# Optimization experiments

Hardware: AMD Instinct MI355X
Metric: run time of the kernel (lower is better)

Reference implementation:

```python
import jax, jax.numpy as jnp
import numpy as np

# --- SLAYER hyperparameters (from netParams) ---
THETA = 10.0        # spike threshold
TAU_SR = 10.0       # SRM alpha-kernel time constant (ms)
TAU_RHO = 1.0       # surrogate-gradient width
SCALE_RHO = 1.0     # surrogate-gradient scale
TS = 1.0            # simulation step (ms)
T_SAMPLE = 300      # number of time steps
K_LEN = 64          # truncated SRM kernel length

N_BATCH, N_IN, N_HID, N_OUT = 128, 784, 410, 10


def srm_kernel():
    # SRM-alpha kernel eps(t) = (t/tau) * exp(1 - t/tau), sampled at Ts, eps(0)=0
    t = jnp.arange(K_LEN, dtype=jnp.float32) * TS
    return (t / TAU_SR) * jnp.exp(1.0 - t / TAU_SR)


def psp(x):
    # Causal FIR filtering along time: out[t] = sum_k eps[k] * x[t-k]
    # x: [N, C, T]
    n, c, t = x.shape
    kern = srm_kernel()
    lhs = x.reshape(n * c, 1, t)
    rhs = kern[::-1].reshape(1, 1, K_LEN)  # flip: conv_general_dilated is cross-correlation
    out = jax.lax.conv_general_dilated(
        lhs, rhs, window_strides=(1,), padding=[(K_LEN - 1, 0)],
        dimension_numbers=("NCH", "OIH", "NCH"))
    return out.reshape(n, c, t)


@jax.custom_vjp
def spike_fn(u):
    # Heaviside threshold with surrogate gradient rho(u) = (scale/tau) * exp(-|u-theta|/tau)
    return (u >= THETA).astype(u.dtype)

def _spike_fwd(u):
    return spike_fn(u), u

def _spike_bwd(u, g):
    return (g * (SCALE_RHO / TAU_RHO) * jnp.exp(-jnp.abs(u - THETA) / TAU_RHO),)

spike_fn.defvjp(_spike_fwd, _spike_bwd)


def setup_inputs() -> dict:
    key = jax.random.key(0)
    k1, k2, k3, k4 = jax.random.split(key, 4)
    img = jax.random.uniform(k1, (N_BATCH, N_IN), dtype=jnp.float32)
    rand_u = jax.random.uniform(k2, (N_BATCH, N_IN, T_SAMPLE), dtype=jnp.float32)
    W1 = jax.random.normal(k3, (N_HID, N_IN), dtype=jnp.float32)
    W2 = jax.random.normal(k4, (N_OUT, N_HID), dtype=jnp.float32)
    return {"img": img, "rand_u": rand_u, "W1": W1, "W2": W2}


def reference(img, rand_u, W1, W2):
    # Poisson spike encoding: spike whenever uniform noise < pixel intensity
    s0 = (rand_u < img[:, :, None]).astype(jnp.float32)        # [N, 784, T]
    # fc1 (dense over spatial features, shared over time) -> psp -> spike
    a1 = jnp.einsum("nit,oi->not", s0, W1)                     # [N, 410, T]
    s1 = spike_fn(psp(a1))
    # fc2 -> psp -> spike
    a2 = jnp.einsum("nht,oh->not", s1, W2)                     # [N, 10, T]
    s2 = spike_fn(psp(a2))
    return s2
```

## Files before the change

### kernel.cpp

```cpp
#include <hip/hip_runtime.h>
#include <cstdint>
#include <cstddef>

#define N_B 128
#define N_I 784
#define N_H 410
#define N_O 10
#define TT  300
#define KL  64
#define NW  26
#define NKS 13
#define NTILES 26
#define NDIG 4
#define NKS2 7
#define S1_TILE 4800
#define S1_NSTRIDE 134400

typedef int v4i __attribute__((ext_vector_type(4)));

__device__ __forceinline__ uint32_t expand4(uint32_t v) {
  return (v * 0x00204081u) & 0x01010101u;
}

__global__ void k_pack(const float* __restrict__ rand_u, const float* __restrict__ img,
                       uint32_t* __restrict__ s0w) {
  int n = blockIdx.y;
  int t = blockIdx.x * 64 + threadIdx.x;
  if (t >= TT) return;
  const float* rb = rand_u + (size_t)n * N_I * TT + t;
  const float* ib = img + (size_t)n * N_I;
  uint32_t* dst = s0w + ((size_t)n * TT + t) * NW;
  #pragma unroll 1
  for (int w = 0; w < 25; ++w) {
    int ib32 = w * 32;
    float r[32];
    #pragma unroll
    for (int b = 0; b < 32; ++b) {
      int i = ib32 + b;
      r[b] = (i < N_I) ? rb[(size_t)i * TT] : 2.0f;
    }
    uint32_t bits = 0;
    #pragma unroll
    for (int b = 0; b < 32; ++b) {
      int i = ib32 + b;
      float p = (i < N_I) ? ib[i] : 0.0f;
      bits |= (r[b] < p ? 1u : 0u) << b;
    }
    dst[w] = bits;
  }
  dst[25] = 0;
}

__global__ void k_bprepall(const float* __restrict__ W1, const float* __restrict__ W2,
                           v4i* __restrict__ Bf, v4i* __restrict__ Bf2) {
  int bid  = blockIdx.x;
  int lane = threadIdx.x;
  if (bid < NDIG * NTILES * NKS) {
    int ks   = bid % NKS;
    int rest = bid / NKS;
    int nt   = rest % NTILES;
    int d    = rest / NTILES;
    int o     = nt * 16 + (lane & 15);
    int kbase = ks * 64 + (lane >> 4) * 16;
    uint32_t wds[4] = {0, 0, 0, 0};
    for (int j = 0; j < 16; ++j) {
      int k = kbase + j;
      int dig = 0;
      if (o < N_H && k < N_I) {
        double w = (double)W1[(size_t)o * N_I + k];
        int r = (int)llround(w * 268435456.0);
        for (int dd = 0; dd <= d; ++dd) {
          dig = (int)(int8_t)(uint8_t)(r & 255);
          r = (r - dig) >> 8;
        }
      }
      wds[j >> 2] |= ((uint32_t)(uint8_t)(int8_t)dig) << (8 * (j & 3));
    }
    v4i v; v[0] = (int)wds[0]; v[1] = (int)wds[1]; v[2] = (int)wds[2]; v[3] = (int)wds[3];
    Bf[(size_t)bid * 64 + lane] = v;
  } else {
    int b2 = bid - NDIG * NTILES * NKS;
    int ks = b2 % NKS2, d = b2 / NKS2;
    int o     = lane & 15;
    int kbase = ks * 64 + (lane >> 4) * 16;
    uint32_t wds[4] = {0, 0, 0, 0};
    for (int j = 0; j < 16; ++j) {
      int k = kbase + j;
      int dig = 0;
      if (o < N_O && k < N_H) {
        double w = (double)W2[(size_t)o * N_H + k];
        int r = (int)llround(w * 268435456.0);
        for (int dd = 0; dd <= d; ++dd) {
          dig = (int)(int8_t)(uint8_t)(r & 255);
          r = (r - dig) >> 8;
        }
      }
      wds[j >> 2] |= ((uint32_t)(uint8_t)(int8_t)dig) << (8 * (j & 3));
    }
    v4i v; v[0] = (int)wds[0]; v[1] = (int)wds[1]; v[2] = (int)wds[2]; v[3] = (int)wds[3];
    Bf2[(size_t)b2 * 64 + lane] = v;
  }
}

__global__ __launch_bounds__(256) void k_fused2(const uint32_t* __restrict__ s0w,
                                                const v4i* __restrict__ Bf,
                                                uint8_t* __restrict__ s1) {
  __shared__ double tile[TT][17];
  int tid = threadIdx.x;
  int wave = tid >> 6, lane = tid & 63;
  int nt = blockIdx.x, n = blockIdx.y;
  int lrow = lane & 15, quad = lane >> 4;
  int wsel = quad >> 1, hsel = (quad & 1) * 16;
  const v4i* bb = Bf + (size_t)nt * NKS * 64 + lane;
  const size_t dstr = (size_t)NTILES * NKS * 64;
  const uint32_t* srow = s0w + (size_t)n * TT * NW;

  v4i acc[5][NDIG];
  #pragma unroll
  for (int mti = 0; mti < 5; ++mti)
    #pragma unroll
    for (int d = 0; d < NDIG; ++d) { acc[mti][d][0]=0; acc[mti][d][1]=0; acc[mti][d][2]=0; acc[mti][d][3]=0; }
  int rowc[5];
  #pragma unroll
  for (int mti = 0; mti < 5; ++mti) {
    int rr = wave * 80 + mti * 16 + lrow;
    rowc[mti] = (rr > TT - 1) ? TT - 1 : rr;
  }
  v4i bcur[NDIG]; uint32_t acur[5];
  #pragma unroll
  for (int d = 0; d < NDIG; ++d) bcur[d] = bb[(size_t)d * dstr];
  #pragma unroll
  for (int mti = 0; mti < 5; ++mti) acur[mti] = srow[(size_t)rowc[mti] * NW + wsel];
  for (int ks = 0; ks < NKS; ++ks) {
    int ks2 = (ks + 1 < NKS) ? ks + 1 : ks;
    v4i bnxt[NDIG]; uint32_t anxt[5];
    #pragma unroll
    for (int d = 0; d < NDIG; ++d) bnxt[d] = bb[(size_t)d * dstr + ks2 * 64];
    #pragma unroll
    for (int mti = 0; mti < 5; ++mti) anxt[mti] = srow[(size_t)rowc[mti] * NW + ks2 * 2 + wsel];
    #pragma unroll
    for (int mti = 0; mti < 5; ++mti) {
      uint32_t h = (acur[mti] >> hsel) & 0xFFFFu;
      v4i af;
      af[0] = (int)expand4(h & 0xF);
      af[1] = (int)expand4((h >> 4) & 0xF);
      af[2] = (int)expand4((h >> 8) & 0xF);
      af[3] = (int)expand4((h >> 12) & 0xF);
      #pragma unroll
      for (int d = 0; d < NDIG; ++d)
        acc[mti][d] = __builtin_amdgcn_mfma_i32_16x16x64_i8(af, bcur[d], acc[mti][d], 0, 0, 0);
    }
    #pragma unroll
    for (int d = 0; d < NDIG; ++d) bcur[d] = bnxt[d];
    #pragma unroll
    for (int mti = 0; mti < 5; ++mti) acur[mti] = anxt[mti];
  }
  #pragma unroll
  for (int mti = 0; mti < 5; ++mti)
    #pragma unroll
    for (int r = 0; r < 4; ++r) {
      int m = wave * 80 + mti * 16 + quad * 4 + r;
      if (m < TT) {
        double v = (double)acc[mti][0][r]
                 + 256.0      * (double)acc[mti][1][r]
                 + 65536.0    * (double)acc[mti][2][r]
                 + 16777216.0 * (double)acc[mti][3][r];
        tile[m][lrow] = v;
      }
    }
  __syncthreads();

  if (lane < 16) {
    int g = wave;
    int T0 = g * 75, T1 = T0 + 75;
    int W = T0 - 63; if (W < 0) W = 0;
    int tB = W + 64, tM = (tB < T1) ? tB : T1;
    const double q   = exp(-0.1);
    const double q64 = exp(-6.4);
    const double cS  = (exp(1.0) / 10.0) * (1.0 / 268435456.0);
    double s1a = 0.0, s2a = 0.0, s1b = 0.0, s2b = 0.0;
    uint8_t* sb = s1 + (size_t)n * S1_NSTRIDE + (size_t)nt * S1_TILE + lane;
    for (int t = W; t < T0; ++t) {
      double xa = tile[t][lane];
      s2a = q * (s2a + s1a);
      s1a = q * s1a + xa;
    }
    for (int t = T0; t < tM; ++t) {
      double xa = tile[t][lane];
      s2a = q * (s2a + s1a);
      s1a = q * s1a + xa;
      sb[(size_t)t * 16] = (cS * s2a >= 10.0) ? 1 : 0;
    }
    for (int t = tM; t < T1; ++t) {
      double xb = tile[t - 64][lane];
      double xa = tile[t][lane];
      s2b = q * (s2b + s1b);
      s1b = q * s1b + xb;
      s2a = q * (s2a + s1a);
      s1a = q * s1a + xa;
      double y = cS * (s2a - q64 * (s2b + 64.0 * s1b));
      sb[(size_t)t * 16] = (y >= 10.0) ? 1 : 0;
    }
  }
}

__global__ __launch_bounds__(256) void k_l2f(const uint8_t* __restrict__ s1,
                                             const v4i* __restrict__ Bf2,
                                             float* __restrict__ out) {
  __shared__ double tile2[TT][11];
  int tid = threadIdx.x;
  int wave = tid >> 6, lane = tid & 63;
  int n = blockIdx.x;
  int lrow = lane & 15, quad = lane >> 4;
  const uint8_t* s1n = s1 + (size_t)n * S1_NSTRIDE;
  for (int mt = wave; mt < 19; mt += 4) {
    int m0 = mt * 16;
    int trow = m0 + lrow; if (trow > TT - 1) trow = TT - 1;
    v4i acc[NDIG];
    #pragma unroll
    for (int d = 0; d < NDIG; ++d) { acc[d][0]=0; acc[d][1]=0; acc[d][2]=0; acc[d][3]=0; }
    for (int ks = 0; ks < NKS2; ++ks) {
      v4i af = *(const v4i*)(s1n + (size_t)(ks * 4 + quad) * S1_TILE + (size_t)trow * 16);
      #pragma unroll
      for (int d = 0; d < NDIG; ++d) {
        v4i bf = Bf2[(size_t)(d * NKS2 + ks) * 64 + lane];
        acc[d] = __builtin_amdgcn_mfma_i32_16x16x64_i8(af, bf, acc[d], 0, 0, 0);
      }
    }
    #pragma unroll
    for (int r = 0; r < 4; ++r) {
      int m = m0 + quad * 4 + r;
      if (m < TT && lrow < N_O) {
        double v = (double)acc[0][r]
                 + 256.0      * (double)acc[1][r]
                 + 65536.0    * (double)acc[2][r]
                 + 16777216.0 * (double)acc[3][r];
        tile2[m][lrow] = v;
      }
    }
  }
  __syncthreads();
  if (lane < N_O) {
    int g = wave;
    int T0 = g * 75, T1 = T0 + 75;
    int W = T0 - 63; if (W < 0) W = 0;
    int tB = W + 64, tM = (tB < T1) ? tB : T1;
    const double q   = exp(-0.1);
    const double q64 = exp(-6.4);
    const double cS  = (exp(1.0) / 10.0) * (1.0 / 268435456.0);
    double s1a = 0.0, s2a = 0.0, s1b = 0.0, s2b = 0.0;
    float* ob = out + (size_t)n * N_O * TT + (size_t)lane * TT;
    for (int t = W; t < T0; ++t) {
      double xa = tile2[t][lane];
      s2a = q * (s2a + s1a);
      s1a = q * s1a + xa;
    }
    for (int t = T0; t < tM; ++t) {
      double xa = tile2[t][lane];
      s2a = q * (s2a + s1a);
      s1a = q * s1a + xa;
      ob[t] = (cS * s2a >= 10.0) ? 1.0f : 0.0f;
    }
    for (int t = tM; t < T1; ++t) {
      double xb = tile2[t - 64][lane];
      double xa = tile2[t][lane];
      s2b = q * (s2b + s1b);
      s1b = q * s1b + xb;
      s2a = q * (s2a + s1a);
      s1a = q * s1a + xa;
      double y = cS * (s2a - q64 * (s2b + 64.0 * s1b));
      ob[t] = (y >= 10.0) ? 1.0f : 0.0f;
    }
  }
}

extern "C" void kernel_launch(void* const* d_in, const int* in_sizes, int n_in,
                              void* d_out, int out_size, void* d_ws, size_t ws_size,
                              hipStream_t stream) {
  const float* img   = (const float*)d_in[0];
  const float* randu = (const float*)d_in[1];
  const float* W1    = (const float*)d_in[2];
  const float* W2    = (const float*)d_in[3];
  float* out = (float*)d_out;

  char* ws = (char*)d_ws;
  size_t off = 0;
  auto alloc = [&](size_t bytes) -> void* {
    void* p = ws + off;
    off = (off + bytes + 511) & ~(size_t)511;
    return p;
  };
  uint32_t* s0w = (uint32_t*)alloc((size_t)N_B * TT * NW * sizeof(uint32_t));
  v4i*      Bf  = (v4i*)     alloc((size_t)NDIG * NTILES * NKS * 64 * 16);
  v4i*      Bf2 = (v4i*)     alloc((size_t)NDIG * NKS2 * 64 * 16);
  uint8_t*  s1  = (uint8_t*) alloc((size_t)N_B * S1_NSTRIDE);
  if (off > ws_size) return;

  k_pack    <<<dim3(5, N_B), 64, 0, stream>>>(randu, img, s0w);
  k_bprepall<<<dim3(NDIG * NTILES * NKS + NDIG * NKS2), 64, 0, stream>>>(W1, W2, Bf, Bf2);
  k_fused2  <<<dim3(NTILES, N_B), 256, 0, stream>>>(s0w, Bf, s1);
  k_l2f     <<<dim3(N_B), 256, 0, stream>>>(s1, Bf2, out);
}
```

Baseline: 362.6 us.

## Spread pack over word blocks and parallelize PSP scan across all threads

k_pack now launches one block per 32-input word (a 3D grid) instead of looping over 25 words per thread, which raises memory-level parallelism for the large rand_u read. The PSP filter stage in both layer kernels now uses all 256 threads, giving 16 time segments of 19 steps per column, instead of 4 segments of 75 steps on 16 lanes. Each segment warms up over a 63-step window, which adds redundant recurrence work but shortens the serial chain. tile2 is widened to 17 columns so all 16 column lanes can index it.

```diff
diff --git a/kernel.cpp b/kernel.cpp
--- a/kernel.cpp
+++ b/kernel.cpp
@@ -15,6 +15,7 @@
 #define NKS2 7
 #define S1_TILE 4800
 #define S1_NSTRIDE 134400
+#define SEGL 19
 
 typedef int v4i __attribute__((ext_vector_type(4)));
 
@@ -24,31 +25,27 @@
 
 __global__ void k_pack(const float* __restrict__ rand_u, const float* __restrict__ img,
                        uint32_t* __restrict__ s0w) {
-  int n = blockIdx.y;
   int t = blockIdx.x * 64 + threadIdx.x;
+  int w = blockIdx.y;
+  int n = blockIdx.z;
   if (t >= TT) return;
   const float* rb = rand_u + (size_t)n * N_I * TT + t;
   const float* ib = img + (size_t)n * N_I;
-  uint32_t* dst = s0w + ((size_t)n * TT + t) * NW;
-  #pragma unroll 1
-  for (int w = 0; w < 25; ++w) {
-    int ib32 = w * 32;
-    float r[32];
-    #pragma unroll
-    for (int b = 0; b < 32; ++b) {
-      int i = ib32 + b;
-      r[b] = (i < N_I) ? rb[(size_t)i * TT] : 2.0f;
-    }
-    uint32_t bits = 0;
-    #pragma unroll
-    for (int b = 0; b < 32; ++b) {
-      int i = ib32 + b;
-      float p = (i < N_I) ? ib[i] : 0.0f;
-      bits |= (r[b] < p ? 1u : 0u) << b;
-    }
-    dst[w] = bits;
-  }
-  dst[25] = 0;
+  int ib32 = w * 32;
+  float r[32];
+  #pragma unroll
+  for (int b = 0; b < 32; ++b) {
+    int i = ib32 + b;
+    r[b] = (i < N_I) ? rb[(size_t)i * TT] : 2.0f;
+  }
+  uint32_t bits = 0;
+  #pragma unroll
+  for (int b = 0; b < 32; ++b) {
+    int i = ib32 + b;
+    float p = (i < N_I) ? ib[i] : 0.0f;
+    bits |= (r[b] < p ? 1u : 0u) << b;
+  }
+  s0w[((size_t)n * TT + t) * NW + w] = bits;
 }
 
 __global__ void k_bprepall(const float* __restrict__ W1, const float* __restrict__ W2,
@@ -170,36 +167,36 @@
     }
   __syncthreads();
 
-  if (lane < 16) {
-    int g = wave;
-    int T0 = g * 75, T1 = T0 + 75;
-    int W = T0 - 63; if (W < 0) W = 0;
-    int tB = W + 64, tM = (tB < T1) ? tB : T1;
+  {
+    int col = tid & 15;
+    int seg = tid >> 4;
+    int T0 = seg * SEGL;
+    int Wc = T0 - 63; if (Wc < 0) Wc = 0;
     const double q   = exp(-0.1);
     const double q64 = exp(-6.4);
     const double cS  = (exp(1.0) / 10.0) * (1.0 / 268435456.0);
     double s1a = 0.0, s2a = 0.0, s1b = 0.0, s2b = 0.0;
-    uint8_t* sb = s1 + (size_t)n * S1_NSTRIDE + (size_t)nt * S1_TILE + lane;
-    for (int t = W; t < T0; ++t) {
-      double xa = tile[t][lane];
+    uint8_t* sb = s1 + (size_t)n * S1_NSTRIDE + (size_t)nt * S1_TILE + col;
+    for (int j = 0; j < 63; ++j) {
+      int t = T0 - 63 + j;
+      int tc = (t < 0) ? 0 : t;
+      double xa = (t >= 0) ? tile[tc][col] : 0.0;
       s2a = q * (s2a + s1a);
       s1a = q * s1a + xa;
     }
-    for (int t = T0; t < tM; ++t) {
-      double xa = tile[t][lane];
-      s2a = q * (s2a + s1a);
-      s1a = q * s1a + xa;
-      sb[(size_t)t * 16] = (cS * s2a >= 10.0) ? 1 : 0;
-    }
-    for (int t = tM; t < T1; ++t) {
-      double xb = tile[t - 64][lane];
-      double xa = tile[t][lane];
+    for (int j = 0; j < SEGL; ++j) {
+      int t = T0 + j;
+      int tc = (t > TT - 1) ? TT - 1 : t;
+      int tb = t - 64;
+      int tbc = (tb < 0) ? 0 : tb;
+      double xa = tile[tc][col];
+      double xb = (tb >= Wc) ? tile[tbc][col] : 0.0;
       s2b = q * (s2b + s1b);
       s1b = q * s1b + xb;
       s2a = q * (s2a + s1a);
       s1a = q * s1a + xa;
       double y = cS * (s2a - q64 * (s2b + 64.0 * s1b));
-      sb[(size_t)t * 16] = (y >= 10.0) ? 1 : 0;
+      if (t < TT) sb[(size_t)t * 16] = (y >= 10.0) ? 1 : 0;
     }
   }
 }
@@ -207,7 +204,7 @@
 __global__ __launch_bounds__(256) void k_l2f(const uint8_t* __restrict__ s1,
                                              const v4i* __restrict__ Bf2,
                                              float* __restrict__ out) {
-  __shared__ double tile2[TT][11];
+  __shared__ double tile2[TT][17];
   int tid = threadIdx.x;
   int wave = tid >> 6, lane = tid & 63;
   int n = blockIdx.x;
@@ -240,36 +237,37 @@
     }
   }
   __syncthreads();
-  if (lane < N_O) {
-    int g = wave;
-    int T0 = g * 75, T1 = T0 + 75;
-    int W = T0 - 63; if (W < 0) W = 0;
-    int tB = W + 64, tM = (tB < T1) ? tB : T1;
+
+  {
+    int col = tid & 15;
+    int seg = tid >> 4;
+    int T0 = seg * SEGL;
+    int Wc = T0 - 63; if (Wc < 0) Wc = 0;
     const double q   = exp(-0.1);
     const double q64 = exp(-6.4);
     const double cS  = (exp(1.0) / 10.0) * (1.0 / 268435456.0);
     double s1a = 0.0, s2a = 0.0, s1b = 0.0, s2b = 0.0;
-    float* ob = out + (size_t)n * N_O * TT + (size_t)lane * TT;
-    for (int t = W; t < T0; ++t) {
-      double xa = tile2[t][lane];
+    float* ob = out + (size_t)n * N_O * TT + (size_t)col * TT;
+    for (int j = 0; j < 63; ++j) {
+      int t = T0 - 63 + j;
+      int tc = (t < 0) ? 0 : t;
+      double xa = (t >= 0) ? tile2[tc][col] : 0.0;
       s2a = q * (s2a + s1a);
       s1a = q * s1a + xa;
     }
-    for (int t = T0; t < tM; ++t) {
-      double xa = tile2[t][lane];
-      s2a = q * (s2a + s1a);
-      s1a = q * s1a + xa;
-      ob[t] = (cS * s2a >= 10.0) ? 1.0f : 0.0f;
-    }
-    for (int t = tM; t < T1; ++t) {
-      double xb = tile2[t - 64][lane];
-      double xa = tile2[t][lane];
+    for (int j = 0; j < SEGL; ++j) {
+      int t = T0 + j;
+      int tc = (t > TT - 1) ? TT - 1 : t;
+      int tb = t - 64;
+      int tbc = (tb < 0) ? 0 : tb;
+      double xa = tile2[tc][col];
+      double xb = (tb >= Wc) ? tile2[tbc][col] : 0.0;
       s2b = q * (s2b + s1b);
       s1b = q * s1b + xb;
       s2a = q * (s2a + s1a);
       s1a = q * s1a + xa;
       double y = cS * (s2a - q64 * (s2b + 64.0 * s1b));
-      ob[t] = (y >= 10.0) ? 1.0f : 0.0f;
+      if (t < TT && col < N_O) ob[t] = (y >= 10.0) ? 1.0f : 0.0f;
     }
   }
 }
@@ -296,7 +294,7 @@
   uint8_t*  s1  = (uint8_t*) alloc((size_t)N_B * S1_NSTRIDE);
   if (off > ws_size) return;
 
-  k_pack    <<<dim3(5, N_B), 64, 0, stream>>>(randu, img, s0w);
+  k_pack    <<<dim3(5, NW, N_B), 64, 0, stream>>>(randu, img, s0w);
   k_bprepall<<<dim3(NDIG * NTILES * NKS + NDIG * NKS2), 64, 0, stream>>>(W1, W2, Bf, Bf2);
   k_fused2  <<<dim3(NTILES, N_B), 256, 0, stream>>>(s0w, Bf, s1);
   k_l2f     <<<dim3(N_B), 256, 0, stream>>>(s1, Bf2, out);
```

Result: faster. 310.8 us (-14.3%).
